# Performance work log

Hardware: AMD Instinct MI355X
Metric: run time of the kernel (lower is better)

## Reference

```python
import jax, jax.numpy as jnp
import numpy as np

N = 50000      # nodes
E = 600000     # edges
D_IN = 128
D_HID = 128
D_OUT = 64
BN_EPS = 1e-5


def _linear(key, fan_in, fan_out):
    s = 1.0 / np.sqrt(fan_in)
    kw, kb = jax.random.split(key)
    W = jax.random.uniform(kw, (fan_in, fan_out), jnp.float32, -s, s)
    b = jax.random.uniform(kb, (fan_out,), jnp.float32, -s, s)
    return W, b


def setup_inputs() -> dict:
    key = jax.random.key(0)
    ks = jax.random.split(key, 6)
    x = jax.random.normal(ks[0], (N, D_IN), jnp.float32)
    edge_index = jax.random.randint(ks[1], (2, E), 0, N, dtype=jnp.int64)
    W1, b1 = _linear(ks[2], D_IN, D_HID)
    W2, b2 = _linear(ks[3], D_HID, D_HID)
    W3, b3 = _linear(ks[4], D_HID, D_OUT)
    g1 = jnp.ones((D_HID,), jnp.float32); be1 = jnp.zeros((D_HID,), jnp.float32)
    g2 = jnp.ones((D_HID,), jnp.float32); be2 = jnp.zeros((D_HID,), jnp.float32)
    return {"x": x, "edge_index": edge_index,
            "W1": W1, "b1": b1, "g1": g1, "be1": be1,
            "W2": W2, "b2": b2, "g2": g2, "be2": be2,
            "W3": W3, "b3": b3}


def _gin_conv(x, src, dst, W, b):
    # GIN aggregation: h_i = (1+eps)*x_i + sum_{j->i} x_j, eps=0, then linear
    agg = jax.ops.segment_sum(x[src], dst, num_segments=N)  # [N, d]
    return (agg + x) @ W + b


def _bn(x, gamma, beta):
    # BatchNorm1d in training mode: batch statistics over nodes
    m = x.mean(axis=0)
    v = x.var(axis=0)
    return (x - m) * jax.lax.rsqrt(v + BN_EPS) * gamma + beta


def reference(x, edge_index, W1, b1, g1, be1, W2, b2, g2, be2, W3, b3):
    src, dst = edge_index[0], edge_index[1]
    h = jax.nn.relu(_bn(_gin_conv(x, src, dst, W1, b1), g1, be1))
    h = jax.nn.relu(_bn(_gin_conv(h, src, dst, W2, b2), g2, be2))
    h = _gin_conv(h, src, dst, W3, b3)
    return jax.nn.log_softmax(h, axis=-1)
```

## Files before the change

kernel.cpp:

```cpp
#include <hip/hip_runtime.h>

#define BN_EPS 1e-5f

typedef __attribute__((ext_vector_type(8))) __bf16 bf16x8;
typedef __attribute__((ext_vector_type(4))) float f32x4;

__device__ __forceinline__ unsigned short f2bf(float f) {
    unsigned int u = __float_as_uint(f);
    u = (u + 0x7fffu + ((u >> 16) & 1u)) >> 16;
    return (unsigned short)u;
}
__device__ __forceinline__ float bfLo(unsigned int w) { return __uint_as_float(w << 16); }
__device__ __forceinline__ float bfHi(unsigned int w) { return __uint_as_float(w & 0xffff0000u); }


__global__ void hist_kernel(const int* __restrict__ dst, int* __restrict__ deg, int E) {
    int e = blockIdx.x * blockDim.x + threadIdx.x;
    if (e < E) atomicAdd(&deg[dst[e]], 1);
}

__global__ void scan_block(const int* __restrict__ deg, int* __restrict__ incl,
                           int* __restrict__ bsum, int N) {
    __shared__ int s[256];
    int i = blockIdx.x * 256 + threadIdx.x;
    int v = (i < N) ? deg[i] : 0;
    s[threadIdx.x] = v;
    __syncthreads();
#pragma unroll
    for (int off = 1; off < 256; off <<= 1) {
        int t = (threadIdx.x >= off) ? s[threadIdx.x - off] : 0;
        __syncthreads();
        s[threadIdx.x] += t;
        __syncthreads();
    }
    if (i < N) incl[i] = s[threadIdx.x];
    if (threadIdx.x == 255) bsum[blockIdx.x] = s[255];
}

__global__ void scan_top(int* __restrict__ bsum, int nb) {
    __shared__ int s[256];
    int v = (threadIdx.x < nb) ? bsum[threadIdx.x] : 0;
    s[threadIdx.x] = v;
    __syncthreads();
#pragma unroll
    for (int off = 1; off < 256; off <<= 1) {
        int t = (threadIdx.x >= off) ? s[threadIdx.x - off] : 0;
        __syncthreads();
        s[threadIdx.x] += t;
        __syncthreads();
    }
    if (threadIdx.x < nb) bsum[threadIdx.x] = s[threadIdx.x] - v;
}

__global__ void finalize_rowptr(const int* __restrict__ deg, const int* __restrict__ incl,
                                const int* __restrict__ boff, int* __restrict__ rowptr,
                                int* __restrict__ pos, int N, int E) {
    int i = blockIdx.x * 256 + threadIdx.x;
    if (i < N) {
        int r = incl[i] - deg[i] + boff[i >> 8];
        rowptr[i] = r;
        pos[i] = r;
    }
    if (i == 0) rowptr[N] = E;
}

__global__ void fill_kernel(const int* __restrict__ src, const int* __restrict__ dst,
                            int* __restrict__ pos, int* __restrict__ col, int E) {
    int e = blockIdx.x * blockDim.x + threadIdx.x;
    if (e < E) {
        int slot = atomicAdd(&pos[dst[e]], 1);
        col[slot] = src[e];
    }
}


__global__ void f32_to_bf16_vec(const float* __restrict__ in, unsigned short* __restrict__ out,
                                int total4) {
    int idx = blockIdx.x * blockDim.x + threadIdx.x;
    int stride = gridDim.x * blockDim.x;
    for (int i = idx; i < total4; i += stride) {
        float4 v = reinterpret_cast<const float4*>(in)[i];
        ushort4 o;
        o.x = f2bf(v.x); o.y = f2bf(v.y); o.z = f2bf(v.z); o.w = f2bf(v.w);
        reinterpret_cast<ushort4*>(out)[i] = o;
    }
}

__global__ void prep_w(const float* __restrict__ W, unsigned short* __restrict__ Wsw, int NOUT) {
    int idx = blockIdx.x * 256 + threadIdx.x;
    if (idx >= 128 * NOUT) return;
    int j = idx & 7;
    int l = (idx >> 3) & 63;
    int q = (idx >> 9) & 3;
    int ct = idx >> 11;
    int k = q * 32 + ((l >> 4) & 3) * 8 + j;
    int c = ct * 16 + (l & 15);
    Wsw[idx] = f2bf(W[(size_t)k * NOUT + c]);
}

__global__ void gather_agg_bf(const unsigned short* __restrict__ h,
                              const int* __restrict__ rowptr, const int* __restrict__ col,
                              unsigned short* __restrict__ agg, int N) {
    int t = blockIdx.x * blockDim.x + threadIdx.x;
    int node = t >> 4;
    if (node >= N) return;
    int part = (t & 15) * 8;
    const int beg = rowptr[node], end = rowptr[node + 1];

    float acc[8];
    {
        uint4 sv = *reinterpret_cast<const uint4*>(h + (size_t)node * 128 + part);
        acc[0] = bfLo(sv.x); acc[1] = bfHi(sv.x);
        acc[2] = bfLo(sv.y); acc[3] = bfHi(sv.y);
        acc[4] = bfLo(sv.z); acc[5] = bfHi(sv.z);
        acc[6] = bfLo(sv.w); acc[7] = bfHi(sv.w);
    }
    int e = beg;
    for (; e + 1 < end; e += 2) {
        int s0 = col[e], s1 = col[e + 1];
        uint4 v0 = *reinterpret_cast<const uint4*>(h + (size_t)s0 * 128 + part);
        uint4 v1 = *reinterpret_cast<const uint4*>(h + (size_t)s1 * 128 + part);
        acc[0] += bfLo(v0.x) + bfLo(v1.x); acc[1] += bfHi(v0.x) + bfHi(v1.x);
        acc[2] += bfLo(v0.y) + bfLo(v1.y); acc[3] += bfHi(v0.y) + bfHi(v1.y);
        acc[4] += bfLo(v0.z) + bfLo(v1.z); acc[5] += bfHi(v0.z) + bfHi(v1.z);
        acc[6] += bfLo(v0.w) + bfLo(v1.w); acc[7] += bfHi(v0.w) + bfHi(v1.w);
    }
    if (e < end) {
        uint4 v0 = *reinterpret_cast<const uint4*>(h + (size_t)col[e] * 128 + part);
        acc[0] += bfLo(v0.x); acc[1] += bfHi(v0.x);
        acc[2] += bfLo(v0.y); acc[3] += bfHi(v0.y);
        acc[4] += bfLo(v0.z); acc[5] += bfHi(v0.z);
        acc[6] += bfLo(v0.w); acc[7] += bfHi(v0.w);
    }
    uint4 o;
    o.x = (unsigned int)f2bf(acc[0]) | ((unsigned int)f2bf(acc[1]) << 16);
    o.y = (unsigned int)f2bf(acc[2]) | ((unsigned int)f2bf(acc[3]) << 16);
    o.z = (unsigned int)f2bf(acc[4]) | ((unsigned int)f2bf(acc[5]) << 16);
    o.w = (unsigned int)f2bf(acc[6]) | ((unsigned int)f2bf(acc[7]) << 16);
    *reinterpret_cast<uint4*>(agg + (size_t)node * 128 + part) = o;
}

template <int NOUT>
__global__ __launch_bounds__(256) void gemm_mfma(const unsigned short* __restrict__ A,
                                                 const unsigned short* __restrict__ Wsw,
                                                 const float* __restrict__ bias,
                                                 float* __restrict__ out, int N) {
    constexpr int NT = NOUT / 16;
    const int lane = threadIdx.x & 63;
    const int w = threadIdx.x >> 6;
    const int r0 = blockIdx.x * 64 + w * 16;
    int arow = r0 + (lane & 15);
    if (arow >= N) arow = N - 1;
    const int kb = lane >> 4;
    const unsigned short* ap = A + (size_t)arow * 128 + kb * 8;

    bf16x8 a[4];
#pragma unroll
    for (int q = 0; q < 4; ++q)
        a[q] = *reinterpret_cast<const bf16x8*>(ap + q * 32);

    f32x4 acc[NT];
#pragma unroll
    for (int ct = 0; ct < NT; ++ct) acc[ct] = (f32x4){0.f, 0.f, 0.f, 0.f};

    const bf16x8* wp = reinterpret_cast<const bf16x8*>(Wsw) + lane;
#pragma unroll
    for (int ct = 0; ct < NT; ++ct) {
#pragma unroll
        for (int q = 0; q < 4; ++q) {
            acc[ct] = __builtin_amdgcn_mfma_f32_16x16x32_bf16(
                a[q], wp[(ct * 4 + q) * 64], acc[ct], 0, 0, 0);
        }
    }

    const int crow0 = r0 + (lane >> 4) * 4;
    const int ccol = lane & 15;
#pragma unroll
    for (int ct = 0; ct < NT; ++ct) {
        int c = ct * 16 + ccol;
        float bv = bias[c];
#pragma unroll
        for (int j = 0; j < 4; ++j) {
            int r = crow0 + j;
            if (r < N) out[(size_t)r * NOUT + c] = acc[ct][j] + bv;
        }
    }
}

__global__ void col_stats(const float* __restrict__ t,
                          float* __restrict__ sums, float* __restrict__ sqs,
                          int total4) {
    __shared__ float s_sum[128], s_sq[128];
    const int tid = threadIdx.x;
    if (tid < 128) { s_sum[tid] = 0.f; s_sq[tid] = 0.f; }
    __syncthreads();
    const int idx0 = blockIdx.x * blockDim.x + tid;
    const int stride = gridDim.x * blockDim.x;
    float sm[4] = {0.f, 0.f, 0.f, 0.f}, sq[4] = {0.f, 0.f, 0.f, 0.f};
    for (int idx = idx0; idx < total4; idx += stride) {
        float4 v = reinterpret_cast<const float4*>(t)[idx];
        sm[0] += v.x; sq[0] += v.x * v.x;
        sm[1] += v.y; sq[1] += v.y * v.y;
        sm[2] += v.z; sq[2] += v.z * v.z;
        sm[3] += v.w; sq[3] += v.w * v.w;
    }
    const int col = (idx0 * 4) & 127;
#pragma unroll
    for (int j = 0; j < 4; ++j) {
        atomicAdd(&s_sum[col + j], sm[j]);
        atomicAdd(&s_sq[col + j], sq[j]);
    }
    __syncthreads();
    if (tid < 128) {
        atomicAdd(&sums[tid], s_sum[tid]);
        atomicAdd(&sqs[tid], s_sq[tid]);
    }
}

__global__ void bn_coef(const float* __restrict__ sums, const float* __restrict__ sqs,
                        const float* __restrict__ g, const float* __restrict__ be,
                        float* __restrict__ a, float* __restrict__ c, float invN) {
    int i = threadIdx.x;
    float m = sums[i] * invN;
    float v = sqs[i] * invN - m * m;
    float inv = rsqrtf(v + BN_EPS);
    float ai = g[i] * inv;
    a[i] = ai;
    c[i] = be[i] - m * ai;
}

__global__ void bn_relu_bf16(const float* __restrict__ t, const float* __restrict__ a,
                             const float* __restrict__ c, unsigned short* __restrict__ h,
                             int total4) {
    const int idx0 = blockIdx.x * blockDim.x + threadIdx.x;
    const int stride = gridDim.x * blockDim.x;
    const int col = (idx0 * 4) & 127;
    const float4 av = *reinterpret_cast<const float4*>(a + col);
    const float4 cv = *reinterpret_cast<const float4*>(c + col);
    for (int idx = idx0; idx < total4; idx += stride) {
        float4 v = reinterpret_cast<const float4*>(t)[idx];
        ushort4 o;
        o.x = f2bf(fmaxf(fmaf(v.x, av.x, cv.x), 0.f));
        o.y = f2bf(fmaxf(fmaf(v.y, av.y, cv.y), 0.f));
        o.z = f2bf(fmaxf(fmaf(v.z, av.z, cv.z), 0.f));
        o.w = f2bf(fmaxf(fmaf(v.w, av.w, cv.w), 0.f));
        reinterpret_cast<ushort4*>(h)[idx] = o;
    }
}

__global__ void log_softmax64(float* __restrict__ out, int N) {
    int row = (blockIdx.x * blockDim.x + threadIdx.x) >> 6;
    int lane = threadIdx.x & 63;
    if (row >= N) return;
    float v = out[(size_t)row * 64 + lane];
    float m = v;
#pragma unroll
    for (int o = 32; o > 0; o >>= 1) m = fmaxf(m, __shfl_xor(m, o));
    float e = __expf(v - m);
    float s = e;
#pragma unroll
    for (int o = 32; o > 0; o >>= 1) s += __shfl_xor(s, o);
    out[(size_t)row * 64 + lane] = v - m - __logf(s);
}

extern "C" void kernel_launch(void* const* d_in, const int* in_sizes, int n_in,
                              void* d_out, int out_size, void* d_ws, size_t ws_size,
                              hipStream_t stream) {
    const float* x   = (const float*)d_in[0];
    const int*   ei  = (const int*)d_in[1];
    const float* W1  = (const float*)d_in[2];
    const float* b1  = (const float*)d_in[3];
    const float* g1  = (const float*)d_in[4];
    const float* be1 = (const float*)d_in[5];
    const float* W2  = (const float*)d_in[6];
    const float* b2  = (const float*)d_in[7];
    const float* g2  = (const float*)d_in[8];
    const float* be2 = (const float*)d_in[9];
    const float* W3  = (const float*)d_in[10];
    const float* b3  = (const float*)d_in[11];

    const int N = in_sizes[0] / 128;
    const int E = in_sizes[1] / 2;
    const int* src = ei;
    const int* dst = ei + E;

    float* f1           = (float*)d_ws;
    unsigned short* hb  = (unsigned short*)(f1 + (size_t)N * 128);
    unsigned short* agb = hb + (size_t)N * 128;
    unsigned short* w1s = agb + (size_t)N * 128;
    unsigned short* w2s = w1s + 128 * 128;
    unsigned short* w3s = w2s + 128 * 128;
    float* sums = (float*)(w3s + 128 * 64);
    float* sqs  = sums + 128;
    float* av   = sqs + 128;
    float* cv   = av + 128;
    int* deg    = (int*)(cv + 128);
    int* pos    = deg + N;
    int* rowptr = pos + N;
    int* bsum   = rowptr + N + 1;
    int* colidx = bsum + 256;

    const int nChunks = (N + 255) / 256;
    const int eBlocks = (E + 255) / 256;
    const int gemmBlocks = (N + 63) / 64;
    const int gatherBlocks = (N * 16 + 255) / 256;
    const int total4 = N * 128 / 4;

    f32_to_bf16_vec<<<2048, 256, 0, stream>>>(x, hb, total4);
    prep_w<<<(128 * 128 + 255) / 256, 256, 0, stream>>>(W1, w1s, 128);
    prep_w<<<(128 * 128 + 255) / 256, 256, 0, stream>>>(W2, w2s, 128);
    prep_w<<<(128 * 64 + 255) / 256, 256, 0, stream>>>(W3, w3s, 64);

    hipMemsetAsync(deg, 0, (size_t)N * sizeof(int), stream);
    hist_kernel<<<eBlocks, 256, 0, stream>>>(dst, deg, E);
    scan_block<<<nChunks, 256, 0, stream>>>(deg, pos, bsum, N);
    scan_top<<<1, 256, 0, stream>>>(bsum, nChunks);
    finalize_rowptr<<<nChunks, 256, 0, stream>>>(deg, pos, bsum, rowptr, pos, N, E);
    fill_kernel<<<eBlocks, 256, 0, stream>>>(src, dst, pos, colidx, E);

    gather_agg_bf<<<gatherBlocks, 256, 0, stream>>>(hb, rowptr, colidx, agb, N);
    gemm_mfma<128><<<gemmBlocks, 256, 0, stream>>>(agb, w1s, b1, f1, N);
    hipMemsetAsync(sums, 0, 2 * 128 * sizeof(float), stream);
    col_stats<<<1024, 256, 0, stream>>>(f1, sums, sqs, total4);
    bn_coef<<<1, 128, 0, stream>>>(sums, sqs, g1, be1, av, cv, 1.0f / N);
    bn_relu_bf16<<<2048, 256, 0, stream>>>(f1, av, cv, hb, total4);

    gather_agg_bf<<<gatherBlocks, 256, 0, stream>>>(hb, rowptr, colidx, agb, N);
    gemm_mfma<128><<<gemmBlocks, 256, 0, stream>>>(agb, w2s, b2, f1, N);
    hipMemsetAsync(sums, 0, 2 * 128 * sizeof(float), stream);
    col_stats<<<1024, 256, 0, stream>>>(f1, sums, sqs, total4);
    bn_coef<<<1, 128, 0, stream>>>(sums, sqs, g2, be2, av, cv, 1.0f / N);
    bn_relu_bf16<<<2048, 256, 0, stream>>>(f1, av, cv, hb, total4);

    gather_agg_bf<<<gatherBlocks, 256, 0, stream>>>(hb, rowptr, colidx, agb, N);
    gemm_mfma<64><<<gemmBlocks, 256, 0, stream>>>(agb, w3s, b3, (float*)d_out, N);
    log_softmax64<<<(N * 64 + 255) / 256, 256, 0, stream>>>((float*)d_out, N);
}
```

Measured before the change: 293.0 us.

## Fuse BN statistics into GEMM epilogue and log-softmax into final GEMM

```diff
diff --git a/kernel.cpp b/kernel.cpp
--- a/kernel.cpp
+++ b/kernel.cpp
@@ -73,29 +73,34 @@
     }
 }
 
-
-__global__ void f32_to_bf16_vec(const float* __restrict__ in, unsigned short* __restrict__ out,
-                                int total4) {
-    int idx = blockIdx.x * blockDim.x + threadIdx.x;
+__global__ void convert_and_prep(const float* __restrict__ x, unsigned short* __restrict__ hb,
+                                 int total4,
+                                 const float* __restrict__ W1, const float* __restrict__ W2,
+                                 const float* __restrict__ W3,
+                                 unsigned short* __restrict__ w1s, unsigned short* __restrict__ w2s,
+                                 unsigned short* __restrict__ w3s) {
+    int tid0 = blockIdx.x * blockDim.x + threadIdx.x;
+    if (tid0 < 40960) {
+        int idx = tid0;
+        const float* W; unsigned short* O; int NOUT;
+        if (idx < 16384)      { W = W1; O = w1s; NOUT = 128; }
+        else if (idx < 32768) { W = W2; O = w2s; NOUT = 128; idx -= 16384; }
+        else                  { W = W3; O = w3s; NOUT = 64;  idx -= 32768; }
+        int j = idx & 7;
+        int l = (idx >> 3) & 63;
+        int q = (idx >> 9) & 3;
+        int ct = idx >> 11;
+        int k = q * 32 + ((l >> 4) & 3) * 8 + j;
+        int c = ct * 16 + (l & 15);
+        O[idx] = f2bf(W[(size_t)k * NOUT + c]);
+    }
     int stride = gridDim.x * blockDim.x;
-    for (int i = idx; i < total4; i += stride) {
-        float4 v = reinterpret_cast<const float4*>(in)[i];
+    for (int i = tid0; i < total4; i += stride) {
+        float4 v = reinterpret_cast<const float4*>(x)[i];
         ushort4 o;
         o.x = f2bf(v.x); o.y = f2bf(v.y); o.z = f2bf(v.z); o.w = f2bf(v.w);
-        reinterpret_cast<ushort4*>(out)[i] = o;
-    }
-}
-
-__global__ void prep_w(const float* __restrict__ W, unsigned short* __restrict__ Wsw, int NOUT) {
-    int idx = blockIdx.x * 256 + threadIdx.x;
-    if (idx >= 128 * NOUT) return;
-    int j = idx & 7;
-    int l = (idx >> 3) & 63;
-    int q = (idx >> 9) & 3;
-    int ct = idx >> 11;
-    int k = q * 32 + ((l >> 4) & 3) * 8 + j;
-    int c = ct * 16 + (l & 15);
-    Wsw[idx] = f2bf(W[(size_t)k * NOUT + c]);
+        reinterpret_cast<ushort4*>(hb)[i] = o;
+    }
 }
 
 __global__ void gather_agg_bf(const unsigned short* __restrict__ h,
@@ -140,12 +145,13 @@
     *reinterpret_cast<uint4*>(agg + (size_t)node * 128 + part) = o;
 }
 
-template <int NOUT>
-__global__ __launch_bounds__(256) void gemm_mfma(const unsigned short* __restrict__ A,
-                                                 const unsigned short* __restrict__ Wsw,
-                                                 const float* __restrict__ bias,
-                                                 float* __restrict__ out, int N) {
-    constexpr int NT = NOUT / 16;
+__global__ __launch_bounds__(256) void gemm128_stats(const unsigned short* __restrict__ A,
+                                                     const unsigned short* __restrict__ Wsw,
+                                                     const float* __restrict__ bias,
+                                                     float* __restrict__ out,
+                                                     float* __restrict__ sumsPad,
+                                                     float* __restrict__ sqsPad, int N) {
+    __shared__ float red[2][4][128];
     const int lane = threadIdx.x & 63;
     const int w = threadIdx.x >> 6;
     const int r0 = blockIdx.x * 64 + w * 16;
@@ -156,111 +162,134 @@
 
     bf16x8 a[4];
 #pragma unroll
-    for (int q = 0; q < 4; ++q)
-        a[q] = *reinterpret_cast<const bf16x8*>(ap + q * 32);
-
-    f32x4 acc[NT];
-#pragma unroll
-    for (int ct = 0; ct < NT; ++ct) acc[ct] = (f32x4){0.f, 0.f, 0.f, 0.f};
+    for (int q = 0; q < 4; ++q) a[q] = *reinterpret_cast<const bf16x8*>(ap + q * 32);
+
+    f32x4 acc[8];
+#pragma unroll
+    for (int ct = 0; ct < 8; ++ct) acc[ct] = (f32x4){0.f, 0.f, 0.f, 0.f};
 
     const bf16x8* wp = reinterpret_cast<const bf16x8*>(Wsw) + lane;
 #pragma unroll
-    for (int ct = 0; ct < NT; ++ct) {
-#pragma unroll
-        for (int q = 0; q < 4; ++q) {
-            acc[ct] = __builtin_amdgcn_mfma_f32_16x16x32_bf16(
-                a[q], wp[(ct * 4 + q) * 64], acc[ct], 0, 0, 0);
-        }
-    }
+    for (int ct = 0; ct < 8; ++ct)
+#pragma unroll
+        for (int q = 0; q < 4; ++q)
+            acc[ct] = __builtin_amdgcn_mfma_f32_16x16x32_bf16(a[q], wp[(ct * 4 + q) * 64],
+                                                              acc[ct], 0, 0, 0);
 
     const int crow0 = r0 + (lane >> 4) * 4;
     const int ccol = lane & 15;
 #pragma unroll
-    for (int ct = 0; ct < NT; ++ct) {
+    for (int ct = 0; ct < 8; ++ct) {
         int c = ct * 16 + ccol;
         float bv = bias[c];
+        float s = 0.f, qq = 0.f;
 #pragma unroll
         for (int j = 0; j < 4; ++j) {
             int r = crow0 + j;
-            if (r < N) out[(size_t)r * NOUT + c] = acc[ct][j] + bv;
+            if (r < N) {
+                float o = acc[ct][j] + bv;
+                out[(size_t)r * 128 + c] = o;
+                s += o; qq += o * o;
+            }
         }
-    }
-}
-
-__global__ void col_stats(const float* __restrict__ t,
-                          float* __restrict__ sums, float* __restrict__ sqs,
-                          int total4) {
-    __shared__ float s_sum[128], s_sq[128];
-    const int tid = threadIdx.x;
-    if (tid < 128) { s_sum[tid] = 0.f; s_sq[tid] = 0.f; }
+        s += __shfl_xor(s, 16); s += __shfl_xor(s, 32);
+        qq += __shfl_xor(qq, 16); qq += __shfl_xor(qq, 32);
+        if (lane < 16) { red[0][w][c] = s; red[1][w][c] = qq; }
+    }
     __syncthreads();
-    const int idx0 = blockIdx.x * blockDim.x + tid;
-    const int stride = gridDim.x * blockDim.x;
-    float sm[4] = {0.f, 0.f, 0.f, 0.f}, sq[4] = {0.f, 0.f, 0.f, 0.f};
-    for (int idx = idx0; idx < total4; idx += stride) {
-        float4 v = reinterpret_cast<const float4*>(t)[idx];
-        sm[0] += v.x; sq[0] += v.x * v.x;
-        sm[1] += v.y; sq[1] += v.y * v.y;
-        sm[2] += v.z; sq[2] += v.z * v.z;
-        sm[3] += v.w; sq[3] += v.w * v.w;
-    }
-    const int col = (idx0 * 4) & 127;
+    int tid = threadIdx.x;
+    if (tid < 128) {
+        float S = red[0][0][tid] + red[0][1][tid] + red[0][2][tid] + red[0][3][tid];
+        atomicAdd(&sumsPad[tid * 16], S);
+    } else {
+        int c = tid - 128;
+        float Q = red[1][0][c] + red[1][1][c] + red[1][2][c] + red[1][3][c];
+        atomicAdd(&sqsPad[c * 16], Q);
+    }
+}
+
+__global__ __launch_bounds__(256) void gemm64_lsm(const unsigned short* __restrict__ A,
+                                                  const unsigned short* __restrict__ Wsw,
+                                                  const float* __restrict__ bias,
+                                                  float* __restrict__ out, int N) {
+    const int lane = threadIdx.x & 63;
+    const int w = threadIdx.x >> 6;
+    const int r0 = blockIdx.x * 64 + w * 16;
+    int arow = r0 + (lane & 15);
+    if (arow >= N) arow = N - 1;
+    const int kb = lane >> 4;
+    const unsigned short* ap = A + (size_t)arow * 128 + kb * 8;
+
+    bf16x8 a[4];
+#pragma unroll
+    for (int q = 0; q < 4; ++q) a[q] = *reinterpret_cast<const bf16x8*>(ap + q * 32);
+
+    f32x4 acc[4];
+#pragma unroll
+    for (int ct = 0; ct < 4; ++ct) acc[ct] = (f32x4){0.f, 0.f, 0.f, 0.f};
+
+    const bf16x8* wp = reinterpret_cast<const bf16x8*>(Wsw) + lane;
+#pragma unroll
+    for (int ct = 0; ct < 4; ++ct)
+#pragma unroll
+        for (int q = 0; q < 4; ++q)
+            acc[ct] = __builtin_amdgcn_mfma_f32_16x16x32_bf16(a[q], wp[(ct * 4 + q) * 64],
+                                                              acc[ct], 0, 0, 0);
+
+    const int crow0 = r0 + (lane >> 4) * 4;
+    const int ccol = lane & 15;
+    float bv[4];
+#pragma unroll
+    for (int ct = 0; ct < 4; ++ct) bv[ct] = bias[ct * 16 + ccol];
+
 #pragma unroll
     for (int j = 0; j < 4; ++j) {
-        atomicAdd(&s_sum[col + j], sm[j]);
-        atomicAdd(&s_sq[col + j], sq[j]);
-    }
-    __syncthreads();
-    if (tid < 128) {
-        atomicAdd(&sums[tid], s_sum[tid]);
-        atomicAdd(&sqs[tid], s_sq[tid]);
-    }
-}
-
-__global__ void bn_coef(const float* __restrict__ sums, const float* __restrict__ sqs,
-                        const float* __restrict__ g, const float* __restrict__ be,
-                        float* __restrict__ a, float* __restrict__ c, float invN) {
-    int i = threadIdx.x;
-    float m = sums[i] * invN;
-    float v = sqs[i] * invN - m * m;
-    float inv = rsqrtf(v + BN_EPS);
-    float ai = g[i] * inv;
-    a[i] = ai;
-    c[i] = be[i] - m * ai;
-}
-
-__global__ void bn_relu_bf16(const float* __restrict__ t, const float* __restrict__ a,
-                             const float* __restrict__ c, unsigned short* __restrict__ h,
-                             int total4) {
+        float o0 = acc[0][j] + bv[0], o1 = acc[1][j] + bv[1];
+        float o2 = acc[2][j] + bv[2], o3 = acc[3][j] + bv[3];
+        float m = fmaxf(fmaxf(o0, o1), fmaxf(o2, o3));
+#pragma unroll
+        for (int off = 1; off < 16; off <<= 1) m = fmaxf(m, __shfl_xor(m, off));
+        float s = __expf(o0 - m) + __expf(o1 - m) + __expf(o2 - m) + __expf(o3 - m);
+#pragma unroll
+        for (int off = 1; off < 16; off <<= 1) s += __shfl_xor(s, off);
+        float ml = m + __logf(s);
+        int r = crow0 + j;
+        if (r < N) {
+            float* op = out + (size_t)r * 64 + ccol;
+            op[0]  = o0 - ml;
+            op[16] = o1 - ml;
+            op[32] = o2 - ml;
+            op[48] = o3 - ml;
+        }
+    }
+}
+
+__global__ void bn_relu_bf16(const float* __restrict__ t, const float* __restrict__ sumsPad,
+                             const float* __restrict__ sqsPad, const float* __restrict__ g,
+                             const float* __restrict__ be, unsigned short* __restrict__ h,
+                             int total4, float invN) {
     const int idx0 = blockIdx.x * blockDim.x + threadIdx.x;
     const int stride = gridDim.x * blockDim.x;
     const int col = (idx0 * 4) & 127;
-    const float4 av = *reinterpret_cast<const float4*>(a + col);
-    const float4 cv = *reinterpret_cast<const float4*>(c + col);
+    float a4[4], c4[4];
+#pragma unroll
+    for (int k = 0; k < 4; ++k) {
+        int c = col + k;
+        float m = sumsPad[c * 16] * invN;
+        float v = sqsPad[c * 16] * invN - m * m;
+        float ai = g[c] * rsqrtf(v + BN_EPS);
+        a4[k] = ai;
+        c4[k] = be[c] - m * ai;
+    }
     for (int idx = idx0; idx < total4; idx += stride) {
         float4 v = reinterpret_cast<const float4*>(t)[idx];
         ushort4 o;
-        o.x = f2bf(fmaxf(fmaf(v.x, av.x, cv.x), 0.f));
-        o.y = f2bf(fmaxf(fmaf(v.y, av.y, cv.y), 0.f));
-        o.z = f2bf(fmaxf(fmaf(v.z, av.z, cv.z), 0.f));
-        o.w = f2bf(fmaxf(fmaf(v.w, av.w, cv.w), 0.f));
+        o.x = f2bf(fmaxf(fmaf(v.x, a4[0], c4[0]), 0.f));
+        o.y = f2bf(fmaxf(fmaf(v.y, a4[1], c4[1]), 0.f));
+        o.z = f2bf(fmaxf(fmaf(v.z, a4[2], c4[2]), 0.f));
+        o.w = f2bf(fmaxf(fmaf(v.w, a4[3], c4[3]), 0.f));
         reinterpret_cast<ushort4*>(h)[idx] = o;
     }
-}
-
-__global__ void log_softmax64(float* __restrict__ out, int N) {
-    int row = (blockIdx.x * blockDim.x + threadIdx.x) >> 6;
-    int lane = threadIdx.x & 63;
-    if (row >= N) return;
-    float v = out[(size_t)row * 64 + lane];
-    float m = v;
-#pragma unroll
-    for (int o = 32; o > 0; o >>= 1) m = fmaxf(m, __shfl_xor(m, o));
-    float e = __expf(v - m);
-    float s = e;
-#pragma unroll
-    for (int o = 32; o > 0; o >>= 1) s += __shfl_xor(s, o);
-    out[(size_t)row * 64 + lane] = v - m - __logf(s);
 }
 
 extern "C" void kernel_launch(void* const* d_in, const int* in_sizes, int n_in,
@@ -288,13 +317,14 @@
     unsigned short* hb  = (unsigned short*)(f1 + (size_t)N * 128);
     unsigned short* agb = hb + (size_t)N * 128;
     unsigned short* w1s = agb + (size_t)N * 128;
-    unsigned short* w2s = w1s + 128 * 128;
-    unsigned short* w3s = w2s + 128 * 128;
-    float* sums = (float*)(w3s + 128 * 64);
-    float* sqs  = sums + 128;
-    float* av   = sqs + 128;
-    float* cv   = av + 128;
-    int* deg    = (int*)(cv + 128);
+    unsigned short* w2s = w1s + 16384;
+    unsigned short* w3s = w2s + 16384;
+    float* statsPad = (float*)(w3s + 8192);
+    float* sums1 = statsPad;
+    float* sqs1  = statsPad + 2048;
+    float* sums2 = statsPad + 4096;
+    float* sqs2  = statsPad + 6144;
+    int* deg    = (int*)(statsPad + 8192);
     int* pos    = deg + N;
     int* rowptr = pos + N;
     int* bsum   = rowptr + N + 1;
@@ -306,12 +336,9 @@
     const int gatherBlocks = (N * 16 + 255) / 256;
     const int total4 = N * 128 / 4;
 
-    f32_to_bf16_vec<<<2048, 256, 0, stream>>>(x, hb, total4);
-    prep_w<<<(128 * 128 + 255) / 256, 256, 0, stream>>>(W1, w1s, 128);
-    prep_w<<<(128 * 128 + 255) / 256, 256, 0, stream>>>(W2, w2s, 128);
-    prep_w<<<(128 * 64 + 255) / 256, 256, 0, stream>>>(W3, w3s, 64);
-
-    hipMemsetAsync(deg, 0, (size_t)N * sizeof(int), stream);
+    hipMemsetAsync(statsPad, 0, 8192 * sizeof(float) + (size_t)N * sizeof(int), stream);
+
+    convert_and_prep<<<2048, 256, 0, stream>>>(x, hb, total4, W1, W2, W3, w1s, w2s, w3s);
     hist_kernel<<<eBlocks, 256, 0, stream>>>(dst, deg, E);
     scan_block<<<nChunks, 256, 0, stream>>>(deg, pos, bsum, N);
     scan_top<<<1, 256, 0, stream>>>(bsum, nChunks);
@@ -319,20 +346,13 @@
     fill_kernel<<<eBlocks, 256, 0, stream>>>(src, dst, pos, colidx, E);
 
     gather_agg_bf<<<gatherBlocks, 256, 0, stream>>>(hb, rowptr, colidx, agb, N);
-    gemm_mfma<128><<<gemmBlocks, 256, 0, stream>>>(agb, w1s, b1, f1, N);
-    hipMemsetAsync(sums, 0, 2 * 128 * sizeof(float), stream);
-    col_stats<<<1024, 256, 0, stream>>>(f1, sums, sqs, total4);
-    bn_coef<<<1, 128, 0, stream>>>(sums, sqs, g1, be1, av, cv, 1.0f / N);
-    bn_relu_bf16<<<2048, 256, 0, stream>>>(f1, av, cv, hb, total4);
+    gemm128_stats<<<gemmBlocks, 256, 0, stream>>>(agb, w1s, b1, f1, sums1, sqs1, N);
+    bn_relu_bf16<<<2048, 256, 0, stream>>>(f1, sums1, sqs1, g1, be1, hb, total4, 1.0f / N);
 
     gather_agg_bf<<<gatherBlocks, 256, 0, stream>>>(hb, rowptr, colidx, agb, N);
-    gemm_mfma<128><<<gemmBlocks, 256, 0, stream>>>(agb, w2s, b2, f1, N);
-    hipMemsetAsync(sums, 0, 2 * 128 * sizeof(float), stream);
-    col_stats<<<1024, 256, 0, stream>>>(f1, sums, sqs, total4);
-    bn_coef<<<1, 128, 0, stream>>>(sums, sqs, g2, be2, av, cv, 1.0f / N);
-    bn_relu_bf16<<<2048, 256, 0, stream>>>(f1, av, cv, hb, total4);
+    gemm128_stats<<<gemmBlocks, 256, 0, stream>>>(agb, w2s, b2, f1, sums2, sqs2, N);
+    bn_relu_bf16<<<2048, 256, 0, stream>>>(f1, sums2, sqs2, g2, be2, hb, total4, 1.0f / N);
 
     gather_agg_bf<<<gatherBlocks, 256, 0, stream>>>(hb, rowptr, colidx, agb, N);
-    gemm_mfma<64><<<gemmBlocks, 256, 0, stream>>>(agb, w3s, b3, (float*)d_out, N);
-    log_softmax64<<<(N * 64 + 255) / 256, 256, 0, stream>>>((float*)d_out, N);
-}
+    gemm64_lsm<<<gemmBlocks, 256, 0, stream>>>(agb, w3s, b3, (float*)d_out, N);
+}
```

Result: faster. 258.3 us (-11.8%).
